# Optimization experiments

Hardware: AMD Instinct MI355X
Metric: run time of the kernel (lower is better)

The kernel has to match this reference:

```python
import jax, jax.numpy as jnp
import numpy as np

B, IN, OUT, TDIM, YDIM = 4096, 48, 64, 128, 64
HID = OUT * OUT  # 4096, Y_layer hidden/output width


def setup_inputs() -> dict:
    key = jax.random.key(0)
    ks = jax.random.split(key, 9)
    x = jax.random.normal(ks[0], (B, IN, IN), dtype=jnp.float32)
    # symmetrize so input is SPD-like (module assumes SPD inputs)
    x = 0.5 * (x + jnp.swapaxes(x, 1, 2))
    t = jax.random.normal(ks[1], (B, TDIM), dtype=jnp.float32)
    Y = jax.random.normal(ks[2], (B, YDIM), dtype=jnp.float32)
    # Stiefel (orthogonal) weight [input_size(=OUT after increase), output_size]
    W, _ = jnp.linalg.qr(jax.random.normal(ks[3], (OUT, OUT), dtype=jnp.float32))
    # Y_layer MLP params: Linear(YDIM,HID) -> SiLU -> Linear(HID,HID)
    Y_W1 = jax.random.normal(ks[4], (YDIM, HID), dtype=jnp.float32) / np.sqrt(YDIM)
    Y_b1 = jnp.zeros((HID,), dtype=jnp.float32)
    Y_W2 = jax.random.normal(ks[5], (HID, HID), dtype=jnp.float32) / np.sqrt(HID)
    Y_b2 = jnp.zeros((HID,), dtype=jnp.float32)
    return {"input": x, "t": t, "Y": Y, "W": W,
            "Y_W1": Y_W1, "Y_b1": Y_b1, "Y_W2": Y_W2, "Y_b2": Y_b2}


def reference(input, t, Y, W, Y_W1, Y_b1, Y_W2, Y_b2):
    # Y_layer MLP -> per-sample transform emb_Y [B, OUT, OUT]
    h = jax.nn.silu(Y @ Y_W1 + Y_b1)
    emb_Y = (h @ Y_W2 + Y_b2).reshape(B, OUT, OUT)
    # SPDIncreaseDim: embed input in top-left of OUTxOUT, ones on padded diagonal
    pad = OUT - IN
    xp = jnp.pad(input, ((0, 0), (0, pad), (0, pad)))
    add_diag = jnp.concatenate([jnp.zeros(IN, input.dtype), jnp.ones(pad, input.dtype)])
    xp = xp + jnp.diag(add_diag)[None]
    # congruence with Stiefel weight: W^T X W
    out = jnp.einsum('ji,bjk,kl->bil', W, xp, W)
    # congruence with MLP-generated weight: emb_Y X emb_Y^T
    out = jnp.einsum('bij,bjk,blk->bil', emb_Y, out, emb_Y)
    return out
```

## Files before the change

### kernel.cpp

```cpp
#include <hip/hip_runtime.h>
#include <hip/hip_bf16.h>

typedef __bf16 bf16;
typedef __bf16 bf16x8 __attribute__((ext_vector_type(8)));
typedef float floatx4 __attribute__((ext_vector_type(4)));
typedef float floatx16 __attribute__((ext_vector_type(16)));

#define MFMA16(a, b, c) __builtin_amdgcn_mfma_f32_16x16x32_bf16((a), (b), (c), 0, 0, 0)
#define MFMA32(a, b, c) __builtin_amdgcn_mfma_f32_32x32x16_bf16((a), (b), (c), 0, 0, 0)

__device__ inline void gload_lds16(const void* g, void* l) {
    __builtin_amdgcn_global_load_lds((__attribute__((address_space(1))) void*)g,
                                     (__attribute__((address_space(3))) void*)l, 16, 0, 0);
}

#define ST 72

__global__ __launch_bounds__(256) void prep_fused(
    const float* __restrict__ W2, const float* __restrict__ W,
    const float* __restrict__ b2, const float* __restrict__ Y,
    const float* __restrict__ W1, const float* __restrict__ b1,
    bf16* __restrict__ W2fT, float* __restrict__ b2f, bf16* __restrict__ h)
{
    __shared__ __align__(16) char smem[45056];
    int t = threadIdx.x, bid = blockIdx.x;
    int w = t >> 6, l = t & 63;
    int lm = l & 15, q2 = l >> 4, q8 = q2 * 8;

    if (bid < 2048) {
        int pt = bid & 31, i = bid >> 5;
        bf16* sW = (bf16*)smem;
        bf16* sA = sW + 64 * 72;
        bf16* sT = sA + 128 * 72;
        int p0 = pt * 128;

#pragma unroll
        for (int kk = 0; kk < 16; kk++) {
            int idx = t + 256 * kk;
            sW[(idx >> 6) * 72 + (idx & 63)] = (bf16)W[idx];
        }
        {
            const float* src = W2 + (size_t)p0 * 4096 + i * 64;
#pragma unroll
            for (int kk = 0; kk < 8; kk++) {
                int c = t + 256 * kk;
                int row = c >> 4, j4 = (c & 15) * 4;
                float4 v = *(const float4*)(src + (size_t)row * 4096 + j4);
                bf16 tmp[4] = {(bf16)v.x, (bf16)v.y, (bf16)v.z, (bf16)v.w};
                *(uint2*)(sA + row * 72 + j4) = *(const uint2*)tmp;
            }
        }
        __syncthreads();

        floatx4 acc[2][4] = {};
#pragma unroll
        for (int kc = 0; kc < 2; kc++) {
            bf16x8 a0 = *(const bf16x8*)(sA + (w * 32 + lm) * 72 + kc * 32 + q8);
            bf16x8 a1 = *(const bf16x8*)(sA + (w * 32 + 16 + lm) * 72 + kc * 32 + q8);
#pragma unroll
            for (int jn = 0; jn < 4; jn++) {
                bf16x8 bf_ = *(const bf16x8*)(sW + (jn * 16 + lm) * 72 + kc * 32 + q8);
                acc[0][jn] = MFMA16(a0, bf_, acc[0][jn]);
                acc[1][jn] = MFMA16(a1, bf_, acc[1][jn]);
            }
        }
#pragma unroll
        for (int im = 0; im < 2; im++)
#pragma unroll
            for (int jn = 0; jn < 4; jn++) {
                int pr = w * 32 + im * 16 + q2 * 4;
                int lc = jn * 16 + lm;
                union { bf16 h4[4]; uint2 u; } pk;
#pragma unroll
                for (int r = 0; r < 4; r++) pk.h4[r] = (bf16)acc[im][jn][r];
                *(uint2*)(sT + lc * 136 + pr) = pk.u;
            }
        __syncthreads();
#pragma unroll
        for (int kk = 0; kk < 4; kk++) {
            int c = t + 256 * kk;
            int row = c >> 4, off = (c & 15) * 8;
            uint4 v = *(const uint4*)(sT + row * 136 + off);
            *(uint4*)(W2fT + (size_t)(i * 64 + row) * 4096 + p0 + off) = v;
        }
        return;
    }

    if (bid < 2112) {
        int i = bid - 2048;
        if (t < 64) {
            float acc = 0.f;
            const float* b2r = b2 + i * 64;
            const float* wr_ = W + t * 64;
#pragma unroll
            for (int j = 0; j < 64; j++) acc = fmaf(b2r[j], wr_[j], acc);
            b2f[i * 64 + t] = acc;
        }
        return;
    }

    {
        int q = bid - 2112;
        int m0 = (q >> 5) * 128, n0 = (q & 31) * 128;
        bf16* sY = (bf16*)smem;
        bf16* sWT = sY + 128 * 72;

#pragma unroll
        for (int kk = 0; kk < 8; kk++) {
            int c = t + 256 * kk;
            int row = c >> 4, c4 = (c & 15) * 4;
            float4 v = *(const float4*)(Y + (size_t)(m0 + row) * 64 + c4);
            bf16 tmp[4] = {(bf16)v.x, (bf16)v.y, (bf16)v.z, (bf16)v.w};
            *(uint2*)(sY + row * 72 + c4) = *(const uint2*)tmp;
        }
#pragma unroll
        for (int kk = 0; kk < 8; kk++) {
            int c = t + 256 * kk;
            int k = c >> 5, j4 = (c & 31) * 4;
            float4 v = *(const float4*)(W1 + (size_t)k * 4096 + n0 + j4);
            sWT[(j4 + 0) * 72 + k] = (bf16)v.x;
            sWT[(j4 + 1) * 72 + k] = (bf16)v.y;
            sWT[(j4 + 2) * 72 + k] = (bf16)v.z;
            sWT[(j4 + 3) * 72 + k] = (bf16)v.w;
        }
        __syncthreads();

        int wn = (w & 1) * 64, wm = (w >> 1) * 64;
        floatx4 acc[4][4] = {};
#pragma unroll
        for (int kc = 0; kc < 2; kc++) {
            bf16x8 af[4], bfr[4];
#pragma unroll
            for (int i = 0; i < 4; i++)
                af[i] = *(const bf16x8*)(sWT + (wn + i * 16 + lm) * 72 + kc * 32 + q8);
#pragma unroll
            for (int j = 0; j < 4; j++)
                bfr[j] = *(const bf16x8*)(sY + (wm + j * 16 + lm) * 72 + kc * 32 + q8);
#pragma unroll
            for (int i = 0; i < 4; i++)
#pragma unroll
                for (int j = 0; j < 4; j++)
                    acc[i][j] = MFMA16(af[i], bfr[j], acc[i][j]);
        }
#pragma unroll
        for (int i = 0; i < 4; i++) {
            int nb = n0 + wn + i * 16 + q2 * 4;
            float4 bv = *(const float4*)(b1 + nb);
            float bb[4] = {bv.x, bv.y, bv.z, bv.w};
#pragma unroll
            for (int j = 0; j < 4; j++) {
                int m = m0 + wm + j * 16 + lm;
                union { bf16 h4[4]; uint2 u; } pk;
#pragma unroll
                for (int r = 0; r < 4; r++) {
                    float v = acc[i][j][r] + bb[r];
                    v = v / (1.f + __expf(-v));
                    pk.h4[r] = (bf16)v;
                }
                *(uint2*)(h + (size_t)m * 4096 + nb) = pk.u;
            }
        }
    }
}

__global__ __launch_bounds__(256, 4) void gemm_bt_bias(
    const bf16* __restrict__ A, const bf16* __restrict__ BT,
    const float* __restrict__ bias, bf16* __restrict__ C)
{
    __shared__ bf16 sA[2][4096];
    __shared__ bf16 sB[2][4096];
    int t = threadIdx.x, w = t >> 6, l = t & 63;
    int bid = blockIdx.x;
    int xcd = bid & 7, local = bid >> 3;
    int mt = xcd * 4 + (local & 3), nt = local >> 2;
    int m0 = mt * 128, n0 = nt * 128;

    int l31 = l & 31, h1 = l >> 5;
    int wr = (w >> 1) * 64, wc = (w & 1) * 64;
    int fo = h1 * 8;

    int rowA = (w * 64 + l) >> 2, ko = (l & 3) * 8;
    const bf16* pa = A + (size_t)(m0 + rowA) * 4096 + ko;
    const bf16* pb = BT + (size_t)(n0 + rowA) * 4096 + ko;
    const int base0 = (w * 64) * 8, base1 = (w * 64 + 256) * 8;

    floatx16 acc[2][2] = {};

    auto issue = [&](int buf, const bf16* a, const bf16* b) {
        gload_lds16(a, &sA[buf][base0]);
        gload_lds16(a + (size_t)64 * 4096, &sA[buf][base1]);
        gload_lds16(b, &sB[buf][base0]);
        gload_lds16(b + (size_t)64 * 4096, &sB[buf][base1]);
    };

    issue(0, pa, pb);
    pa += 32; pb += 32;
    __syncthreads();

    for (int kt = 0; kt < 128; ++kt) {
        int cur = kt & 1;
        if (kt + 1 < 128) {
            issue(cur ^ 1, pa, pb);
            pa += 32; pb += 32;
        }
        const bf16* LA = sA[cur];
        const bf16* LB = sB[cur];
        bf16x8 a0[2], a1[2], b0[2], b1[2];
#pragma unroll
        for (int i = 0; i < 2; i++) {
            a0[i] = *(const bf16x8*)(LA + (wr + i * 32 + l31) * 32 + fo);
            a1[i] = *(const bf16x8*)(LA + (wr + i * 32 + l31) * 32 + fo + 16);
            b0[i] = *(const bf16x8*)(LB + (wc + i * 32 + l31) * 32 + fo);
            b1[i] = *(const bf16x8*)(LB + (wc + i * 32 + l31) * 32 + fo + 16);
        }
#pragma unroll
        for (int i = 0; i < 2; i++)
#pragma unroll
            for (int j = 0; j < 2; j++) {
                acc[i][j] = MFMA32(a0[i], b0[j], acc[i][j]);
                acc[i][j] = MFMA32(a1[i], b1[j], acc[i][j]);
            }
        __syncthreads();
    }

#pragma unroll
    for (int j = 0; j < 2; j++) {
        int cc = n0 + wc + j * 32 + l31;
        float bb = bias[cc];
#pragma unroll
        for (int i = 0; i < 2; i++) {
            int rbase = m0 + wr + i * 32 + 4 * h1;
#pragma unroll
            for (int g = 0; g < 4; g++)
#pragma unroll
                for (int r2 = 0; r2 < 4; r2++)
                    C[(size_t)(rbase + 8 * g + r2) * 4096 + cc] =
                        (bf16)(acc[i][j][4 * g + r2] + bb);
        }
    }
}

__global__ __launch_bounds__(256) void batched_congruence(
    const float* __restrict__ x, const bf16* __restrict__ F,
    float* __restrict__ out)
{
    __shared__ bf16 sX[64 * ST], sF[64 * ST], sT[64 * ST];
    int t = threadIdx.x, w = t >> 6, l = t & 63;
    int b = blockIdx.x;
    int lm = l & 15, q2 = l >> 4, q8 = q2 * 8;
    int r0 = (w >> 1) * 32, c0 = (w & 1) * 32;

    const float4* xb = (const float4*)(x + (size_t)b * 2304);
    float4 v0 = xb[t];
    float4 v1 = xb[t + 256];
    float4 v2 = (t < 64) ? xb[t + 512] : make_float4(0.f, 0.f, 0.f, 0.f);
    {
        const uint4* gf = (const uint4*)(F + (size_t)b * 4096);
#pragma unroll
        for (int kk = 0; kk < 2; kk++) {
            int c = t + 256 * kk;
            *(uint4*)(sF + (c >> 3) * ST + (c & 7) * 8) = gf[c];
        }
    }
    {
        unsigned* sx32 = (unsigned*)sX;
#pragma unroll
        for (int kk = 0; kk < 4; kk++) {
            int idx = t + 256 * kk;
            if (idx < 384) {
                int r = idx >> 3, d = 24 + (idx & 7);
                sx32[r * 36 + d] = 0u;
            } else if (idx < 896) {
                int k2 = idx - 384;
                int r = 48 + (k2 >> 5), d = k2 & 31;
                unsigned val = 0u;
                if (d == (r >> 1)) val = (r & 1) ? 0x3F800000u : 0x00003F80u;
                sx32[r * 36 + d] = val;
            }
        }
    }
    {
        int c = t;
        bf16 p4[4];
        p4[0] = (bf16)v0.x; p4[1] = (bf16)v0.y; p4[2] = (bf16)v0.z; p4[3] = (bf16)v0.w;
        *(uint2*)(sX + (c / 12) * ST + (c % 12) * 4) = *(const uint2*)p4;
        c = t + 256;
        p4[0] = (bf16)v1.x; p4[1] = (bf16)v1.y; p4[2] = (bf16)v1.z; p4[3] = (bf16)v1.w;
        *(uint2*)(sX + (c / 12) * ST + (c % 12) * 4) = *(const uint2*)p4;
        if (t < 64) {
            c = t + 512;
            p4[0] = (bf16)v2.x; p4[1] = (bf16)v2.y; p4[2] = (bf16)v2.z; p4[3] = (bf16)v2.w;
            *(uint2*)(sX + (c / 12) * ST + (c % 12) * 4) = *(const uint2*)p4;
        }
    }
    __syncthreads();

    auto mm = [&](const bf16* PA, const bf16* PB, floatx4 acc[2][2]) {
#pragma unroll
        for (int kc = 0; kc < 2; kc++) {
            bf16x8 a0 = *(const bf16x8*)(PA + (r0 + lm) * ST + kc * 32 + q8);
            bf16x8 a1 = *(const bf16x8*)(PA + (r0 + 16 + lm) * ST + kc * 32 + q8);
            bf16x8 b0 = *(const bf16x8*)(PB + (c0 + lm) * ST + kc * 32 + q8);
            bf16x8 b1 = *(const bf16x8*)(PB + (c0 + 16 + lm) * ST + kc * 32 + q8);
            acc[0][0] = MFMA16(a0, b0, acc[0][0]);
            acc[0][1] = MFMA16(a0, b1, acc[0][1]);
            acc[1][0] = MFMA16(a1, b0, acc[1][0]);
            acc[1][1] = MFMA16(a1, b1, acc[1][1]);
        }
    };

    floatx4 z = {0.f, 0.f, 0.f, 0.f};
    {
        floatx4 a2[2][2] = {{z, z}, {z, z}};
        mm(sX, sF, a2);
#pragma unroll
        for (int i = 0; i < 2; i++)
#pragma unroll
            for (int j = 0; j < 2; j++) {
                int R = r0 + i * 16 + q2 * 4;
                int Cc = c0 + j * 16 + lm;
                union { bf16 h4[4]; uint2 u; } pk;
#pragma unroll
                for (int r = 0; r < 4; r++) pk.h4[r] = (bf16)a2[i][j][r];
                *(uint2*)(sT + Cc * ST + R) = pk.u;
            }
    }
    __syncthreads();
    {
        floatx4 a3[2][2] = {{z, z}, {z, z}};
        mm(sT, sF, a3);
        float* ob = out + (size_t)b * 4096;
#pragma unroll
        for (int i = 0; i < 2; i++)
#pragma unroll
            for (int j = 0; j < 2; j++) {
                int R = r0 + i * 16 + q2 * 4;
                int Cc = c0 + j * 16 + lm;
                float4 vout = make_float4(a3[i][j][0], a3[i][j][1], a3[i][j][2], a3[i][j][3]);
                *(float4*)(ob + Cc * 64 + R) = vout;
            }
    }
}

extern "C" void kernel_launch(void* const* d_in, const int* in_sizes, int n_in,
                              void* d_out, int out_size, void* d_ws, size_t ws_size,
                              hipStream_t stream) {
    const float* x  = (const float*)d_in[0];
    const float* Y  = (const float*)d_in[2];
    const float* W  = (const float*)d_in[3];
    const float* W1 = (const float*)d_in[4];
    const float* b1 = (const float*)d_in[5];
    const float* W2 = (const float*)d_in[6];
    const float* b2 = (const float*)d_in[7];
    float* out = (float*)d_out;

    const size_t NN = (size_t)4096 * 4096;
    bf16* h    = (bf16*)d_ws;
    bf16* W2fT = h + NN;
    bf16* emb  = W2fT + NN;
    float* b2f = (float*)d_out;

    prep_fused<<<3136, 256, 0, stream>>>(W2, W, b2, Y, W1, b1, W2fT, b2f, h);
    gemm_bt_bias<<<1024, 256, 0, stream>>>(h, W2fT, b2f, emb);
    batched_congruence<<<4096, 256, 0, stream>>>(x, emb, out);
}
```

Baseline: 358.2 us.

## Switch GEMM to 16x16x32 MFMA with XOR-swizzled LDS layout, reorder prep blocks

```diff
diff --git a/kernel.cpp b/kernel.cpp
--- a/kernel.cpp
+++ b/kernel.cpp
@@ -4,10 +4,8 @@
 typedef __bf16 bf16;
 typedef __bf16 bf16x8 __attribute__((ext_vector_type(8)));
 typedef float floatx4 __attribute__((ext_vector_type(4)));
-typedef float floatx16 __attribute__((ext_vector_type(16)));
 
 #define MFMA16(a, b, c) __builtin_amdgcn_mfma_f32_16x16x32_bf16((a), (b), (c), 0, 0, 0)
-#define MFMA32(a, b, c) __builtin_amdgcn_mfma_f32_32x32x16_bf16((a), (b), (c), 0, 0, 0)
 
 __device__ inline void gload_lds16(const void* g, void* l) {
     __builtin_amdgcn_global_load_lds((__attribute__((address_space(1))) void*)g,
@@ -28,7 +26,7 @@
     int lm = l & 15, q2 = l >> 4, q8 = q2 * 8;
 
     if (bid < 2048) {
-        int pt = bid & 31, i = bid >> 5;
+        int i = bid & 63, pt = bid >> 6;
         bf16* sW = (bf16*)smem;
         bf16* sA = sW + 64 * 72;
         bf16* sT = sA + 128 * 72;
@@ -174,68 +172,54 @@
     int xcd = bid & 7, local = bid >> 3;
     int mt = xcd * 4 + (local & 3), nt = local >> 2;
     int m0 = mt * 128, n0 = nt * 128;
-
-    int l31 = l & 31, h1 = l >> 5;
+    int lm = l & 15, q2 = l >> 4;
+    int soff = ((q2 - (l & 3)) & 3) * 8;
     int wr = (w >> 1) * 64, wc = (w & 1) * 64;
-    int fo = h1 * 8;
-
-    int rowA = (w * 64 + l) >> 2, ko = (l & 3) * 8;
+    int rowA = (w * 64 + l) >> 2;
+    int ko = (((l & 3) + rowA) & 3) * 8;
     const bf16* pa = A + (size_t)(m0 + rowA) * 4096 + ko;
     const bf16* pb = BT + (size_t)(n0 + rowA) * 4096 + ko;
     const int base0 = (w * 64) * 8, base1 = (w * 64 + 256) * 8;
 
-    floatx16 acc[2][2] = {};
-
+    floatx4 acc[4][4] = {};
     auto issue = [&](int buf, const bf16* a, const bf16* b) {
         gload_lds16(a, &sA[buf][base0]);
         gload_lds16(a + (size_t)64 * 4096, &sA[buf][base1]);
         gload_lds16(b, &sB[buf][base0]);
         gload_lds16(b + (size_t)64 * 4096, &sB[buf][base1]);
     };
-
     issue(0, pa, pb);
     pa += 32; pb += 32;
     __syncthreads();
-
     for (int kt = 0; kt < 128; ++kt) {
         int cur = kt & 1;
-        if (kt + 1 < 128) {
-            issue(cur ^ 1, pa, pb);
-            pa += 32; pb += 32;
-        }
+        if (kt + 1 < 128) { issue(cur ^ 1, pa, pb); pa += 32; pb += 32; }
         const bf16* LA = sA[cur];
         const bf16* LB = sB[cur];
-        bf16x8 a0[2], a1[2], b0[2], b1[2];
-#pragma unroll
-        for (int i = 0; i < 2; i++) {
-            a0[i] = *(const bf16x8*)(LA + (wr + i * 32 + l31) * 32 + fo);
-            a1[i] = *(const bf16x8*)(LA + (wr + i * 32 + l31) * 32 + fo + 16);
-            b0[i] = *(const bf16x8*)(LB + (wc + i * 32 + l31) * 32 + fo);
-            b1[i] = *(const bf16x8*)(LB + (wc + i * 32 + l31) * 32 + fo + 16);
-        }
-#pragma unroll
-        for (int i = 0; i < 2; i++)
-#pragma unroll
-            for (int j = 0; j < 2; j++) {
-                acc[i][j] = MFMA32(a0[i], b0[j], acc[i][j]);
-                acc[i][j] = MFMA32(a1[i], b1[j], acc[i][j]);
-            }
+        bf16x8 af[4], bfr[4];
+#pragma unroll
+        for (int i = 0; i < 4; i++)
+            af[i] = *(const bf16x8*)(LA + (wr + i * 16 + lm) * 32 + soff);
+#pragma unroll
+        for (int j = 0; j < 4; j++)
+            bfr[j] = *(const bf16x8*)(LB + (wc + j * 16 + lm) * 32 + soff);
+#pragma unroll
+        for (int i = 0; i < 4; i++)
+#pragma unroll
+            for (int j = 0; j < 4; j++)
+                acc[i][j] = MFMA16(af[i], bfr[j], acc[i][j]);
         __syncthreads();
     }
-
-#pragma unroll
-    for (int j = 0; j < 2; j++) {
-        int cc = n0 + wc + j * 32 + l31;
-        float bb = bias[cc];
-#pragma unroll
-        for (int i = 0; i < 2; i++) {
-            int rbase = m0 + wr + i * 32 + 4 * h1;
-#pragma unroll
-            for (int g = 0; g < 4; g++)
-#pragma unroll
-                for (int r2 = 0; r2 < 4; r2++)
-                    C[(size_t)(rbase + 8 * g + r2) * 4096 + cc] =
-                        (bf16)(acc[i][j][4 * g + r2] + bb);
+#pragma unroll
+    for (int i = 0; i < 4; i++) {
+        int r0 = m0 + wr + i * 16 + q2 * 4;
+#pragma unroll
+        for (int j = 0; j < 4; j++) {
+            int cc = n0 + wc + j * 16 + lm;
+            float bb = bias[cc];
+#pragma unroll
+            for (int r = 0; r < 4; r++)
+                C[(size_t)(r0 + r) * 4096 + cc] = (bf16)(acc[i][j][r] + bb);
         }
     }
 }
```

New measurement: 335.5 us. 6.4% less time.
